# Performance work log

Hardware: AMD Instinct MI355X
Metric: run time of the kernel (lower is better)

The kernel has to match this reference:

```python
import jax, jax.numpy as jnp
import numpy as np

B, L, D = 8192, 200, 64
NUM_ITEMS = 100000
HID = 64  # attention hidden_dim


def setup_inputs() -> dict:
    key = jax.random.key(0)
    ks = jax.random.split(key, 16)
    inp = {
        "item_sequence": jax.random.randint(ks[0], (B, L), 0, NUM_ITEMS),
        "click_sequence": jax.random.randint(ks[1], (B, L), 0, 2),
        "seq_length": jax.random.randint(ks[2], (B, 1), 1, L + 1),
        "target_item": jax.random.randint(ks[3], (B, 1), 0, NUM_ITEMS),
        "context_features": jax.random.normal(ks[4], (B, 9), dtype=jnp.float32),
        # embedding table (num_items+1, D)
        "emb_table": jax.random.normal(ks[5], (NUM_ITEMS + 1, D), dtype=jnp.float32) * 0.05,
        # attention MLP: Linear(2D->64), Linear(64->32), Linear(32->1)
        "aw1": jax.random.normal(ks[6], (2 * D, HID), dtype=jnp.float32) * 0.05,
        "ab1": jnp.zeros((HID,), jnp.float32),
        "aw2": jax.random.normal(ks[7], (HID, HID // 2), dtype=jnp.float32) * 0.05,
        "ab2": jnp.zeros((HID // 2,), jnp.float32),
        "aw3": jax.random.normal(ks[8], (HID // 2, 1), dtype=jnp.float32) * 0.05,
        "ab3": jnp.zeros((1,), jnp.float32),
        # context MLP: Linear(9->32)
        "cw": jax.random.normal(ks[9], (9, 32), dtype=jnp.float32) * 0.05,
        "cb": jnp.zeros((32,), jnp.float32),
        # head MLP: Linear(160->128), Linear(128->64), Linear(64->1)
        "mw1": jax.random.normal(ks[10], (2 * D + 32, 128), dtype=jnp.float32) * 0.05,
        "mb1": jnp.zeros((128,), jnp.float32),
        "mw2": jax.random.normal(ks[11], (128, 64), dtype=jnp.float32) * 0.05,
        "mb2": jnp.zeros((64,), jnp.float32),
        "mw3": jax.random.normal(ks[12], (64, 1), dtype=jnp.float32) * 0.05,
        "mb3": jnp.zeros((1,), jnp.float32),
    }
    return inp


def reference(item_sequence, click_sequence, seq_length, target_item, context_features,
              emb_table, aw1, ab1, aw2, ab2, aw3, ab3, cw, cb,
              mw1, mb1, mw2, mb2, mw3, mb3):
    seq_emb = emb_table[item_sequence]                 # [B, L, D]
    tgt_emb = emb_table[target_item[:, 0]]             # [B, D]
    seq_len = item_sequence.shape[1]
    mask = (jnp.arange(seq_len)[None, :] < seq_length).astype(seq_emb.dtype)  # [B, L]

    # DIN attention: concat(query, keys) -> 3-layer MLP -> masked softmax -> weighted sum
    q = jnp.broadcast_to(tgt_emb[:, None, :], seq_emb.shape)          # [B, L, D]
    att_in = jnp.concatenate([q, seq_emb], axis=-1)                   # [B, L, 2D]
    h = jax.nn.relu(att_in @ aw1 + ab1)
    h = jax.nn.relu(h @ aw2 + ab2)
    scores = (h @ aw3 + ab3)[..., 0]                                  # [B, L]
    scores = jnp.where(mask == 0, jnp.asarray(-1e9, scores.dtype), scores)
    w = jax.nn.softmax(scores, axis=1)                                # [B, L]
    attended = jnp.einsum('bl,bld->bd', w, seq_emb)                   # [B, D]

    ctx = jax.nn.relu(context_features @ cw + cb)                     # [B, 32]
    comb = jnp.concatenate([attended, tgt_emb, ctx], axis=1)          # [B, 2D+32]
    h = jax.nn.relu(comb @ mw1 + mb1)
    h = jax.nn.relu(h @ mw2 + mb2)
    out = jax.nn.sigmoid(h @ mw3 + mb3)[:, 0]                         # [B]
    return out
```

## Files before the change

### kernel.cpp

```cpp
#include <hip/hip_runtime.h>
#include <cmath>

typedef __attribute__((ext_vector_type(8))) short s16x8;
typedef __attribute__((ext_vector_type(4))) short s16x4;
typedef __attribute__((ext_vector_type(4))) float f32x4;

__device__ __forceinline__ short f2bf(float f) {
    union { float f; unsigned u; } v; v.f = f;
    unsigned r = v.u + 0x7FFFu + ((v.u >> 16) & 1u);
    return (short)(r >> 16);
}
__device__ __forceinline__ float bf2f(short s) {
    union { unsigned u; float f; } v; v.u = ((unsigned)(unsigned short)s) << 16;
    return v.f;
}

#define EMB_ELEMS 6400064
#define W1SEQ_SH  6400064
#define W1TOP_SH  6404160
#define W2_SH     6408256
#define MW1T_SH   6410304
#define MW2T_SH   6430784
#define CB_SH     10764352

__global__ __launch_bounds__(256)
void din_prep_kernel(const float* __restrict__ emb,
                     const float* __restrict__ aw1,
                     const float* __restrict__ aw2,
                     const float* __restrict__ mw1,
                     const float* __restrict__ mw2,
                     short* __restrict__ ws)
{
    const int bid = blockIdx.x;
    const int t = threadIdx.x;
    if (bid < 6251) {
        long e4 = ((long)bid * 256 + t) * 4;
        if (e4 < EMB_ELEMS) {
            float4 v = *(const float4*)(emb + e4);
            s16x4 bv = { f2bf(v.x), f2bf(v.y), f2bf(v.z), f2bf(v.w) };
            *(s16x4*)(ws + e4) = bv;
        }
        return;
    }
    const int wb = bid - 6251;
    if (wb == 0) {
        for (int idx = t; idx < 4096; idx += 256) {
            int j = idx & 7, lane = (idx >> 3) & 63, fr = idx >> 9;
            int n = (fr >> 1) * 16 + (lane & 15);
            int k = (fr & 1) * 32 + (lane >> 4) * 8 + j;
            ws[W1SEQ_SH + idx] = f2bf(aw1[(64 + k) * 64 + n]);
        }
    } else if (wb == 1) {
        for (int idx = t; idx < 4096; idx += 256) {
            int j = idx & 7, lane = (idx >> 3) & 63, fr = idx >> 9;
            int n = (fr >> 1) * 16 + (lane & 15);
            int k = (fr & 1) * 32 + (lane >> 4) * 8 + j;
            ws[W1TOP_SH + idx] = f2bf(aw1[k * 64 + n]);
        }
    } else if (wb == 2) {
        for (int idx = t; idx < 2048; idx += 256) {
            int j = idx & 7, lane = (idx >> 3) & 63, fr = idx >> 9;
            int n = (fr >> 1) * 16 + (lane & 15);
            int k = (fr & 1) * 32 + (lane >> 4) * 8 + j;
            ws[W2_SH + idx] = f2bf(aw2[k * 32 + n]);
        }
    } else if (wb == 3) {
        for (int idx = t; idx < 8192; idx += 256) {
            int j = idx & 7, lane = (idx >> 3) & 63, fr = idx >> 9;
            int n = (fr >> 2) * 16 + (lane & 15);
            int k = (fr & 3) * 32 + (lane >> 4) * 8 + j;
            ws[MW2T_SH + idx] = f2bf(mw2[k * 64 + n]);
        }
    } else {
        const int base = (wb - 4) * 5120;
        for (int ii = t; ii < 5120; ii += 256) {
            int idx = base + ii;
            int j = idx & 7, lane = (idx >> 3) & 63, fr = idx >> 9;
            int nt = fr / 5, ks = fr - nt * 5;
            int n = nt * 16 + (lane & 15);
            int k = ks * 32 + (lane >> 4) * 8 + j;
            ws[MW1T_SH + idx] = f2bf(mw1[k * 128 + n]);
        }
    }
}

#define H1_PITCH 72
__global__ __launch_bounds__(256)
void din_att_v2(const int* __restrict__ item_seq,
                const int* __restrict__ seq_len_p,
                const int* __restrict__ tgt_item,
                const float* __restrict__ ctx_feat,
                const float* __restrict__ ab1,
                const float* __restrict__ ab2,
                const float* __restrict__ aw3, const float* __restrict__ ab3,
                const float* __restrict__ cw,  const float* __restrict__ cb,
                short* __restrict__ ws)
{
    const int t = threadIdx.x, lane = t & 63, wave = t >> 6;
    const int quad = lane >> 4, r16 = lane & 15;
    __shared__ short s_wall[10240];
    __shared__ short s_h1[4][16 * H1_PITCH];
    __shared__ float s_sc[4][64];
    __shared__ float s_pool[4][64];
    __shared__ float s_m[4], s_e[4];

    const int b   = blockIdx.x;
    const int len = seq_len_p[b];
    const int tgt = tgt_item[b];
    const short* embbf = ws;

    {
        const s16x8* src = (const s16x8*)(ws + W1SEQ_SH);
        s16x8* dst = (s16x8*)s_wall;
        #pragma unroll
        for (int i = 0; i < 2; ++i) dst[t + i * 256] = src[t + i * 256];
        if (t < 128) dst[t + 512] = src[t + 512];
    }

    bool act[4];
    s16x8 af[4][2];
    #pragma unroll
    for (int ci = 0; ci < 4; ++ci) {
        const int c = wave + ci * 4;
        act[ci] = (c < 13) && (c * 16 < len);
        if (act[ci]) {
            int r = c * 16 + r16; if (r > 199) r = 199;
            const int it = item_seq[b * 200 + r];
            af[ci][0] = *(const s16x8*)(embbf + it * 64 + quad * 8);
            af[ci][1] = *(const s16x8*)(embbf + it * 64 + 32 + quad * 8);
        }
    }
    s16x8 at0 = {}, at1 = {};
    if (r16 == 0) {
        at0 = *(const s16x8*)(embbf + tgt * 64 + quad * 8);
        at1 = *(const s16x8*)(embbf + tgt * 64 + 32 + quad * 8);
    }
    __syncthreads();

    float qcv[4];
    {
        f32x4 qacc[4] = {{0,0,0,0},{0,0,0,0},{0,0,0,0},{0,0,0,0}};
        #pragma unroll
        for (int nt = 0; nt < 4; ++nt) {
            s16x8 b_0 = *(const s16x8*)&s_wall[4096 + ((nt * 2 + 0) * 64 + lane) * 8];
            s16x8 b_1 = *(const s16x8*)&s_wall[4096 + ((nt * 2 + 1) * 64 + lane) * 8];
            qacc[nt] = __builtin_amdgcn_mfma_f32_16x16x32_bf16(at0, b_0, qacc[nt], 0, 0, 0);
            qacc[nt] = __builtin_amdgcn_mfma_f32_16x16x32_bf16(at1, b_1, qacc[nt], 0, 0, 0);
        }
        #pragma unroll
        for (int nt = 0; nt < 4; ++nt)
            qcv[nt] = __shfl(qacc[nt][0], r16) + ab1[nt * 16 + r16];
    }
    s16x8 w2r[4];
    #pragma unroll
    for (int fr = 0; fr < 4; ++fr)
        w2r[fr] = *(const s16x8*)&s_wall[8192 + (fr * 64 + lane) * 8];
    const float bias2_lo = ab2[r16], bias2_hi = ab2[16 + r16];
    const float w3_lo    = aw3[r16], w3_hi    = aw3[16 + r16];
    const float b3       = ab3[0];
    short* h1w = s_h1[wave];

    #pragma unroll
    for (int ci = 0; ci < 4; ++ci) {
        if (!act[ci]) continue;
        f32x4 acc[4] = {{0,0,0,0},{0,0,0,0},{0,0,0,0},{0,0,0,0}};
        #pragma unroll
        for (int nt = 0; nt < 4; ++nt) {
            s16x8 b_0 = *(const s16x8*)&s_wall[((nt * 2 + 0) * 64 + lane) * 8];
            s16x8 b_1 = *(const s16x8*)&s_wall[((nt * 2 + 1) * 64 + lane) * 8];
            acc[nt] = __builtin_amdgcn_mfma_f32_16x16x32_bf16(af[ci][0], b_0, acc[nt], 0, 0, 0);
            acc[nt] = __builtin_amdgcn_mfma_f32_16x16x32_bf16(af[ci][1], b_1, acc[nt], 0, 0, 0);
        }
        #pragma unroll
        for (int nt = 0; nt < 4; ++nt)
            #pragma unroll
            for (int rr = 0; rr < 4; ++rr) {
                float v = fmaxf(acc[nt][rr] + qcv[nt], 0.f);
                h1w[(quad * 4 + rr) * H1_PITCH + nt * 16 + r16] = f2bf(v);
            }
        __builtin_amdgcn_wave_barrier();

        s16x8 h0  = *(const s16x8*)&h1w[r16 * H1_PITCH + quad * 8];
        s16x8 h1v = *(const s16x8*)&h1w[r16 * H1_PITCH + 32 + quad * 8];
        f32x4 c2[2] = {{0,0,0,0},{0,0,0,0}};
        #pragma unroll
        for (int nt = 0; nt < 2; ++nt) {
            c2[nt] = __builtin_amdgcn_mfma_f32_16x16x32_bf16(h0,  w2r[nt * 2],     c2[nt], 0, 0, 0);
            c2[nt] = __builtin_amdgcn_mfma_f32_16x16x32_bf16(h1v, w2r[nt * 2 + 1], c2[nt], 0, 0, 0);
        }
        #pragma unroll
        for (int rr = 0; rr < 4; ++rr) {
            float p = fmaxf(c2[0][rr] + bias2_lo, 0.f) * w3_lo
                    + fmaxf(c2[1][rr] + bias2_hi, 0.f) * w3_hi;
            p += __shfl_xor(p, 8);
            p += __shfl_xor(p, 4);
            p += __shfl_xor(p, 2);
            p += __shfl_xor(p, 1);
            if (r16 == 0) s_sc[wave][ci * 16 + quad * 4 + rr] = p + b3;
        }
        __builtin_amdgcn_wave_barrier();
    }

    const int ci_l = lane >> 4;
    const int c_l  = wave + ci_l * 4;
    const int grow = c_l * 16 + r16;
    const bool valid = (c_l < 13) && (grow < len);
    float sc = valid ? s_sc[wave][lane] : -1e30f;
    float m = sc;
    #pragma unroll
    for (int off = 32; off; off >>= 1) m = fmaxf(m, __shfl_xor(m, off));
    float e = valid ? __expf(sc - m) : 0.f;
    #pragma unroll
    for (int off = 32; off; off >>= 1) e += __shfl_xor(e, off);

    float p[16];
    #pragma unroll
    for (int i = 0; i < 16; ++i) p[i] = 0.f;
    #pragma unroll
    for (int ci = 0; ci < 4; ++ci) {
        if (!act[ci]) continue;
        const int row = (wave + ci * 4) * 16 + r16;
        const float w = (row < len) ? __expf(s_sc[wave][ci * 16 + r16] - m) : 0.f;
        #pragma unroll
        for (int j = 0; j < 8; ++j) {
            p[j]     += w * bf2f(af[ci][0][j]);
            p[8 + j] += w * bf2f(af[ci][1][j]);
        }
    }
    #pragma unroll
    for (int i = 0; i < 16; ++i) {
        p[i] += __shfl_xor(p[i], 1);
        p[i] += __shfl_xor(p[i], 2);
        p[i] += __shfl_xor(p[i], 4);
        p[i] += __shfl_xor(p[i], 8);
    }
    if (r16 == 0) {
        #pragma unroll
        for (int j = 0; j < 8; ++j) {
            s_pool[wave][quad * 8 + j]      = p[j];
            s_pool[wave][32 + quad * 8 + j] = p[8 + j];
        }
    }
    if (lane == 0) { s_m[wave] = m; s_e[wave] = e; }
    __syncthreads();

    short* comb = ws + CB_SH + b * 160;
    if (t < 64) {
        float gm = fmaxf(fmaxf(s_m[0], s_m[1]), fmaxf(s_m[2], s_m[3]));
        float s0 = __expf(s_m[0] - gm), s1 = __expf(s_m[1] - gm);
        float s2 = __expf(s_m[2] - gm), s3 = __expf(s_m[3] - gm);
        float denom = s0 * s_e[0] + s1 * s_e[1] + s2 * s_e[2] + s3 * s_e[3];
        float pooled = s0 * s_pool[0][t] + s1 * s_pool[1][t]
                     + s2 * s_pool[2][t] + s3 * s_pool[3][t];
        comb[t] = f2bf(pooled / denom);
    } else if (t < 96) {
        const int j = t - 64;
        float a = cb[j];
        #pragma unroll
        for (int k = 0; k < 9; ++k) a += ctx_feat[b * 9 + k] * cw[k * 32 + j];
        comb[128 + j] = f2bf(fmaxf(a, 0.f));
    } else if (t < 160) {
        comb[64 + (t - 96)] = embbf[tgt * 64 + (t - 96)];
    }
}

__global__ __launch_bounds__(64)
void din_mlp_kernel(const float* __restrict__ mb1,
                    const float* __restrict__ mb2,
                    const float* __restrict__ mw3, const float* __restrict__ mb3,
                    const short* __restrict__ ws,
                    float* __restrict__ out)
{
    const int lane = threadIdx.x & 63;
    const int quad = lane >> 4, r16 = lane & 15;
    __shared__ short s_h1[16 * 136];
    __shared__ short s_h2[16 * 72];

    const int b0 = blockIdx.x * 16;
    const short* comb = ws + CB_SH;
    const short* w1   = ws + MW1T_SH;
    const short* w2   = ws + MW2T_SH;

    s16x8 a[5];
    #pragma unroll
    for (int ks = 0; ks < 5; ++ks)
        a[ks] = *(const s16x8*)(comb + (b0 + r16) * 160 + ks * 32 + quad * 8);
    f32x4 acc[8] = {{0,0,0,0},{0,0,0,0},{0,0,0,0},{0,0,0,0},{0,0,0,0},{0,0,0,0},{0,0,0,0},{0,0,0,0}};
    #pragma unroll
    for (int nt = 0; nt < 8; ++nt)
        #pragma unroll
        for (int ks = 0; ks < 5; ++ks) {
            s16x8 bf = *(const s16x8*)(w1 + ((nt * 5 + ks) * 64 + lane) * 8);
            acc[nt] = __builtin_amdgcn_mfma_f32_16x16x32_bf16(a[ks], bf, acc[nt], 0, 0, 0);
        }
    #pragma unroll
    for (int nt = 0; nt < 8; ++nt) {
        float bias = mb1[nt * 16 + r16];
        #pragma unroll
        for (int rr = 0; rr < 4; ++rr)
            s_h1[(quad * 4 + rr) * 136 + nt * 16 + r16] = f2bf(fmaxf(acc[nt][rr] + bias, 0.f));
    }
    __builtin_amdgcn_wave_barrier();

    s16x8 a2[4];
    #pragma unroll
    for (int ks = 0; ks < 4; ++ks)
        a2[ks] = *(const s16x8*)&s_h1[r16 * 136 + ks * 32 + quad * 8];
    f32x4 acc2[4] = {{0,0,0,0},{0,0,0,0},{0,0,0,0},{0,0,0,0}};
    #pragma unroll
    for (int nt = 0; nt < 4; ++nt)
        #pragma unroll
        for (int ks = 0; ks < 4; ++ks) {
            s16x8 bf = *(const s16x8*)(w2 + ((nt * 4 + ks) * 64 + lane) * 8);
            acc2[nt] = __builtin_amdgcn_mfma_f32_16x16x32_bf16(a2[ks], bf, acc2[nt], 0, 0, 0);
        }
    #pragma unroll
    for (int nt = 0; nt < 4; ++nt) {
        float bias = mb2[nt * 16 + r16];
        #pragma unroll
        for (int rr = 0; rr < 4; ++rr)
            s_h2[(quad * 4 + rr) * 72 + nt * 16 + r16] = f2bf(fmaxf(acc2[nt][rr] + bias, 0.f));
    }
    __builtin_amdgcn_wave_barrier();

    float p = 0.f;
    #pragma unroll
    for (int j = 0; j < 16; ++j)
        p += bf2f(s_h2[r16 * 72 + quad * 16 + j]) * mw3[quad * 16 + j];
    p += __shfl_xor(p, 16);
    p += __shfl_xor(p, 32);
    if (quad == 0) out[b0 + r16] = 1.f / (1.f + __expf(-(p + mb3[0])));
}

extern "C" void kernel_launch(void* const* d_in, const int* in_sizes, int n_in,
                              void* d_out, int out_size, void* d_ws, size_t ws_size,
                              hipStream_t stream)
{
    const int*   item_seq  = (const int*)  d_in[0];
    const int*   seq_len   = (const int*)  d_in[2];
    const int*   tgt_item  = (const int*)  d_in[3];
    const float* ctx_feat  = (const float*)d_in[4];
    const float* emb       = (const float*)d_in[5];
    const float* aw1 = (const float*)d_in[6];
    const float* ab1 = (const float*)d_in[7];
    const float* aw2 = (const float*)d_in[8];
    const float* ab2 = (const float*)d_in[9];
    const float* aw3 = (const float*)d_in[10];
    const float* ab3 = (const float*)d_in[11];
    const float* cw  = (const float*)d_in[12];
    const float* cb  = (const float*)d_in[13];
    const float* mw1 = (const float*)d_in[14];
    const float* mb1 = (const float*)d_in[15];
    const float* mw2 = (const float*)d_in[16];
    const float* mb2 = (const float*)d_in[17];
    const float* mw3 = (const float*)d_in[18];
    const float* mb3 = (const float*)d_in[19];
    float* out = (float*)d_out;
    short* ws  = (short*)d_ws;

    hipLaunchKernelGGL(din_prep_kernel, dim3(6259), dim3(256), 0, stream,
                       emb, aw1, aw2, mw1, mw2, ws);
    hipLaunchKernelGGL(din_att_v2, dim3(8192), dim3(256), 0, stream,
                       item_seq, seq_len, tgt_item, ctx_feat,
                       ab1, ab2, aw3, ab3, cw, cb, ws);
    hipLaunchKernelGGL(din_mlp_kernel, dim3(512), dim3(64), 0, stream,
                       mb1, mb2, mw3, mb3, ws, out);
}
```

Before: 196.9 us.

## Drop full embedding-table bf16 conversion; gather fp32 rows and precompute target projection

The prep kernel no longer converts the whole 100k x 64 embedding table to bf16. The attention kernel now gathers fp32 rows directly and converts them in registers. The target-side first-layer projection moves into a separate small MFMA kernel that writes per-batch fp32 bias vectors, which the attention kernel reads. This removes a large read and write pass over the table, at the cost of doubling the bytes per gathered row and adding a kernel launch. W2 is now read from global memory into registers instead of shared memory.

After: 192.4 us. 1.02x faster.

```diff
diff --git a/kernel.cpp b/kernel.cpp
--- a/kernel.cpp
+++ b/kernel.cpp
@@ -14,35 +14,29 @@
     union { unsigned u; float f; } v; v.u = ((unsigned)(unsigned short)s) << 16;
     return v.f;
 }
-
-#define EMB_ELEMS 6400064
-#define W1SEQ_SH  6400064
-#define W1TOP_SH  6404160
-#define W2_SH     6408256
-#define MW1T_SH   6410304
-#define MW2T_SH   6430784
-#define CB_SH     10764352
+__device__ __forceinline__ s16x8 cvt8(float4 a, float4 b) {
+    s16x8 r = { f2bf(a.x), f2bf(a.y), f2bf(a.z), f2bf(a.w),
+                f2bf(b.x), f2bf(b.y), f2bf(b.z), f2bf(b.w) };
+    return r;
+}
+
+#define W1SEQ_SH  0
+#define W1TOP_SH  4096
+#define W2_SH     8192
+#define MW1T_SH   10240
+#define MW2T_SH   30720
+#define QC_F      19456
+#define CB_SH     1087488
 
 __global__ __launch_bounds__(256)
-void din_prep_kernel(const float* __restrict__ emb,
-                     const float* __restrict__ aw1,
-                     const float* __restrict__ aw2,
-                     const float* __restrict__ mw1,
-                     const float* __restrict__ mw2,
-                     short* __restrict__ ws)
-{
-    const int bid = blockIdx.x;
+void din_wprep_kernel(const float* __restrict__ aw1,
+                      const float* __restrict__ aw2,
+                      const float* __restrict__ mw1,
+                      const float* __restrict__ mw2,
+                      short* __restrict__ ws)
+{
+    const int wb = blockIdx.x;
     const int t = threadIdx.x;
-    if (bid < 6251) {
-        long e4 = ((long)bid * 256 + t) * 4;
-        if (e4 < EMB_ELEMS) {
-            float4 v = *(const float4*)(emb + e4);
-            s16x4 bv = { f2bf(v.x), f2bf(v.y), f2bf(v.z), f2bf(v.w) };
-            *(s16x4*)(ws + e4) = bv;
-        }
-        return;
-    }
-    const int wb = bid - 6251;
     if (wb == 0) {
         for (int idx = t; idx < 4096; idx += 256) {
             int j = idx & 7, lane = (idx >> 3) & 63, fr = idx >> 9;
@@ -84,13 +78,49 @@
     }
 }
 
+__global__ __launch_bounds__(256)
+void din_qc_kernel(const int* __restrict__ tgt_item,
+                   const float* __restrict__ emb,
+                   const float* __restrict__ ab1,
+                   short* __restrict__ ws)
+{
+    const int t = threadIdx.x, lane = t & 63, wave = t >> 6;
+    const int quad = lane >> 4, r16 = lane & 15;
+    const short* w1t = ws + W1TOP_SH;
+    float* qc = (float*)ws + QC_F;
+
+    const int b0 = (blockIdx.x * 4 + wave) * 16;
+    const int it = tgt_item[b0 + r16];
+    const float* rp = emb + it * 64 + quad * 8;
+    float4 v0 = *(const float4*)(rp),      v1 = *(const float4*)(rp + 4);
+    float4 v2 = *(const float4*)(rp + 32), v3 = *(const float4*)(rp + 36);
+    s16x8 a0 = cvt8(v0, v1);
+    s16x8 a1 = cvt8(v2, v3);
+
+    f32x4 acc[4] = {{0,0,0,0},{0,0,0,0},{0,0,0,0},{0,0,0,0}};
+    #pragma unroll
+    for (int nt = 0; nt < 4; ++nt) {
+        s16x8 b_0 = *(const s16x8*)(w1t + ((nt * 2 + 0) * 64 + lane) * 8);
+        s16x8 b_1 = *(const s16x8*)(w1t + ((nt * 2 + 1) * 64 + lane) * 8);
+        acc[nt] = __builtin_amdgcn_mfma_f32_16x16x32_bf16(a0, b_0, acc[nt], 0, 0, 0);
+        acc[nt] = __builtin_amdgcn_mfma_f32_16x16x32_bf16(a1, b_1, acc[nt], 0, 0, 0);
+    }
+    #pragma unroll
+    for (int nt = 0; nt < 4; ++nt) {
+        float bias = ab1[nt * 16 + r16];
+        #pragma unroll
+        for (int rr = 0; rr < 4; ++rr)
+            qc[(b0 + quad * 4 + rr) * 64 + nt * 16 + r16] = acc[nt][rr] + bias;
+    }
+}
+
 #define H1_PITCH 72
 __global__ __launch_bounds__(256)
-void din_att_v2(const int* __restrict__ item_seq,
+void din_att_v3(const int* __restrict__ item_seq,
                 const int* __restrict__ seq_len_p,
                 const int* __restrict__ tgt_item,
                 const float* __restrict__ ctx_feat,
-                const float* __restrict__ ab1,
+                const float* __restrict__ emb,
                 const float* __restrict__ ab2,
                 const float* __restrict__ aw3, const float* __restrict__ ab3,
                 const float* __restrict__ cw,  const float* __restrict__ cb,
@@ -98,7 +128,7 @@
 {
     const int t = threadIdx.x, lane = t & 63, wave = t >> 6;
     const int quad = lane >> 4, r16 = lane & 15;
-    __shared__ short s_wall[10240];
+    __shared__ short s_w1[4096];
     __shared__ short s_h1[4][16 * H1_PITCH];
     __shared__ float s_sc[4][64];
     __shared__ float s_pool[4][64];
@@ -107,14 +137,12 @@
     const int b   = blockIdx.x;
     const int len = seq_len_p[b];
     const int tgt = tgt_item[b];
-    const short* embbf = ws;
 
     {
         const s16x8* src = (const s16x8*)(ws + W1SEQ_SH);
-        s16x8* dst = (s16x8*)s_wall;
-        #pragma unroll
-        for (int i = 0; i < 2; ++i) dst[t + i * 256] = src[t + i * 256];
-        if (t < 128) dst[t + 512] = src[t + 512];
+        s16x8* dst = (s16x8*)s_w1;
+        dst[t]       = src[t];
+        dst[t + 256] = src[t + 256];
     }
 
     bool act[4];
@@ -126,38 +154,26 @@
         if (act[ci]) {
             int r = c * 16 + r16; if (r > 199) r = 199;
             const int it = item_seq[b * 200 + r];
-            af[ci][0] = *(const s16x8*)(embbf + it * 64 + quad * 8);
-            af[ci][1] = *(const s16x8*)(embbf + it * 64 + 32 + quad * 8);
-        }
-    }
-    s16x8 at0 = {}, at1 = {};
-    if (r16 == 0) {
-        at0 = *(const s16x8*)(embbf + tgt * 64 + quad * 8);
-        at1 = *(const s16x8*)(embbf + tgt * 64 + 32 + quad * 8);
-    }
-    __syncthreads();
-
+            const float* rp = emb + it * 64 + quad * 8;
+            float4 v0 = *(const float4*)(rp),      v1 = *(const float4*)(rp + 4);
+            float4 v2 = *(const float4*)(rp + 32), v3 = *(const float4*)(rp + 36);
+            af[ci][0] = cvt8(v0, v1);
+            af[ci][1] = cvt8(v2, v3);
+        }
+    }
+    s16x8 w2r[4];
+    #pragma unroll
+    for (int fr = 0; fr < 4; ++fr)
+        w2r[fr] = *(const s16x8*)(ws + W2_SH + (fr * 64 + lane) * 8);
+    const float* qcp = (const float*)ws + QC_F + b * 64;
     float qcv[4];
-    {
-        f32x4 qacc[4] = {{0,0,0,0},{0,0,0,0},{0,0,0,0},{0,0,0,0}};
-        #pragma unroll
-        for (int nt = 0; nt < 4; ++nt) {
-            s16x8 b_0 = *(const s16x8*)&s_wall[4096 + ((nt * 2 + 0) * 64 + lane) * 8];
-            s16x8 b_1 = *(const s16x8*)&s_wall[4096 + ((nt * 2 + 1) * 64 + lane) * 8];
-            qacc[nt] = __builtin_amdgcn_mfma_f32_16x16x32_bf16(at0, b_0, qacc[nt], 0, 0, 0);
-            qacc[nt] = __builtin_amdgcn_mfma_f32_16x16x32_bf16(at1, b_1, qacc[nt], 0, 0, 0);
-        }
-        #pragma unroll
-        for (int nt = 0; nt < 4; ++nt)
-            qcv[nt] = __shfl(qacc[nt][0], r16) + ab1[nt * 16 + r16];
-    }
-    s16x8 w2r[4];
-    #pragma unroll
-    for (int fr = 0; fr < 4; ++fr)
-        w2r[fr] = *(const s16x8*)&s_wall[8192 + (fr * 64 + lane) * 8];
+    #pragma unroll
+    for (int nt = 0; nt < 4; ++nt) qcv[nt] = qcp[nt * 16 + r16];
     const float bias2_lo = ab2[r16], bias2_hi = ab2[16 + r16];
     const float w3_lo    = aw3[r16], w3_hi    = aw3[16 + r16];
     const float b3       = ab3[0];
+    __syncthreads();
+
     short* h1w = s_h1[wave];
 
     #pragma unroll
@@ -166,8 +182,8 @@
         f32x4 acc[4] = {{0,0,0,0},{0,0,0,0},{0,0,0,0},{0,0,0,0}};
         #pragma unroll
         for (int nt = 0; nt < 4; ++nt) {
-            s16x8 b_0 = *(const s16x8*)&s_wall[((nt * 2 + 0) * 64 + lane) * 8];
-            s16x8 b_1 = *(const s16x8*)&s_wall[((nt * 2 + 1) * 64 + lane) * 8];
+            s16x8 b_0 = *(const s16x8*)&s_w1[((nt * 2 + 0) * 64 + lane) * 8];
+            s16x8 b_1 = *(const s16x8*)&s_w1[((nt * 2 + 1) * 64 + lane) * 8];
             acc[nt] = __builtin_amdgcn_mfma_f32_16x16x32_bf16(af[ci][0], b_0, acc[nt], 0, 0, 0);
             acc[nt] = __builtin_amdgcn_mfma_f32_16x16x32_bf16(af[ci][1], b_1, acc[nt], 0, 0, 0);
         }
@@ -260,7 +276,7 @@
         for (int k = 0; k < 9; ++k) a += ctx_feat[b * 9 + k] * cw[k * 32 + j];
         comb[128 + j] = f2bf(fmaxf(a, 0.f));
     } else if (t < 160) {
-        comb[64 + (t - 96)] = embbf[tgt * 64 + (t - 96)];
+        comb[64 + (t - 96)] = f2bf(emb[tgt * 64 + (t - 96)]);
     }
 }
 
@@ -358,11 +374,13 @@
     float* out = (float*)d_out;
     short* ws  = (short*)d_ws;
 
-    hipLaunchKernelGGL(din_prep_kernel, dim3(6259), dim3(256), 0, stream,
-                       emb, aw1, aw2, mw1, mw2, ws);
-    hipLaunchKernelGGL(din_att_v2, dim3(8192), dim3(256), 0, stream,
-                       item_seq, seq_len, tgt_item, ctx_feat,
-                       ab1, ab2, aw3, ab3, cw, cb, ws);
+    hipLaunchKernelGGL(din_wprep_kernel, dim3(8), dim3(256), 0, stream,
+                       aw1, aw2, mw1, mw2, ws);
+    hipLaunchKernelGGL(din_qc_kernel, dim3(128), dim3(256), 0, stream,
+                       tgt_item, emb, ab1, ws);
+    hipLaunchKernelGGL(din_att_v3, dim3(8192), dim3(256), 0, stream,
+                       item_seq, seq_len, tgt_item, ctx_feat, emb,
+                       ab2, aw3, ab3, cw, cb, ws);
     hipLaunchKernelGGL(din_mlp_kernel, dim3(512), dim3(64), 0, stream,
                        mb1, mb2, mw3, mb3, ws, out);
 }
```
